# Kernel optimization log

Measured on AMD Instinct MI355X. Metric: run time of the kernel, lower is better.

Reference implementation:

```python
import jax, jax.numpy as jnp
import numpy as np

EPS = 1e-5

def layer_norm(x, g, b):
    mu = jnp.mean(x, axis=-1, keepdims=True)
    var = jnp.mean(jnp.square(x - mu), axis=-1, keepdims=True)
    return (x - mu) * jax.lax.rsqrt(var + EPS) * g + b

def setup_inputs() -> dict:
    key = jax.random.key(0)
    ks = jax.random.split(key, 16)
    B, S, D, H, T = 8, 1024, 512, 8, 6
    Dff = 4 * D
    s = 0.02
    return {
        "x": jax.random.normal(ks[0], (B, S, D), jnp.float32),
        "signal_type_ids": jax.random.randint(ks[1], (B, S), 0, T, jnp.int32),
        "emb": jax.random.normal(ks[2], (T, D), jnp.float32) * s,
        "in_proj_w": jax.random.normal(ks[3], (3 * D, D), jnp.float32) * s,
        "in_proj_b": jnp.zeros((3 * D,), jnp.float32),
        "out_proj_w": jax.random.normal(ks[4], (D, D), jnp.float32) * s,
        "out_proj_b": jnp.zeros((D,), jnp.float32),
        "ln1_g": jnp.ones((D,), jnp.float32),
        "ln1_b": jnp.zeros((D,), jnp.float32),
        "ln2_g": jnp.ones((D,), jnp.float32),
        "ln2_b": jnp.zeros((D,), jnp.float32),
        "w1": jax.random.normal(ks[5], (Dff, D), jnp.float32) * s,
        "b1": jnp.zeros((Dff,), jnp.float32),
        "w2": jax.random.normal(ks[6], (D, Dff), jnp.float32) * s,
        "b2": jnp.zeros((D,), jnp.float32),
    }

def reference(x, signal_type_ids, emb, in_proj_w, in_proj_b, out_proj_w, out_proj_b,
              ln1_g, ln1_b, ln2_g, ln2_b, w1, b1, w2, b2):
    B, S, D = x.shape
    H = 8
    hd = D // H
    # embedding add
    x = x + emb[signal_type_ids]
    # pre-norm MHA (need_weights=True path, average_attn_weights=True)
    xn = layer_norm(x, ln1_g, ln1_b)
    qkv = xn @ in_proj_w.T + in_proj_b            # [B,S,3D]
    q, k, v = jnp.split(qkv, 3, axis=-1)
    q = q.reshape(B, S, H, hd)
    k = k.reshape(B, S, H, hd)
    v = v.reshape(B, S, H, hd)
    scores = jnp.einsum("bqhd,bkhd->bhqk", q, k) / jnp.sqrt(jnp.asarray(hd, x.dtype))
    attn = jax.nn.softmax(scores, axis=-1)        # [B,H,S,S]
    attn_weights = jnp.mean(attn, axis=1)         # averaged over heads [B,S,S]
    ctx = jnp.einsum("bhqk,bkhd->bqhd", attn, v).reshape(B, S, D)
    attn_out = ctx @ out_proj_w.T + out_proj_b
    x = x + attn_out
    # FFN with exact GELU (torch nn.GELU default)
    h = layer_norm(x, ln2_g, ln2_b)
    h = jax.nn.gelu(h @ w1.T + b1, approximate=False)
    x = x + h @ w2.T + b2
    return x, attn_weights
```

## Files before the change

### kernel.cpp

```cpp
#include <hip/hip_runtime.h>
#include <math.h>

constexpr int CB = 8;
constexpr int CS = 1024;
constexpr int CD = 512;
constexpr int CH = 8;
constexpr int CHD = 64;
constexpr int CDFF = 2048;
constexpr int NROW = CB * CS;

typedef unsigned short u16;
typedef unsigned int u32;
typedef __attribute__((ext_vector_type(8))) short short8;
typedef __attribute__((ext_vector_type(8))) unsigned short ushort8v;
typedef __attribute__((ext_vector_type(4))) float floatx4;

__device__ inline u16 f2bf(float f) {
    union { float f; unsigned u; } v; v.f = f;
    unsigned u = v.u + 0x7FFFu + ((v.u >> 16) & 1u);
    return (u16)(u >> 16);
}
__device__ inline float bf2f(u16 h) {
    union { unsigned u; float f; } v; v.u = ((unsigned)h) << 16;
    return v.f;
}

__device__ inline float gelu_fast(float v) {
    float u = v * (1.0f + 0.044715f * v * v);
    float e = __expf(-1.5957691216057308f * u);
    return v / (1.0f + e);
}

__device__ inline void gload16(const u16* g, u16* l) {
    __builtin_amdgcn_global_load_lds(
        (const __attribute__((address_space(1))) u32*)g,
        (__attribute__((address_space(3))) u32*)l, 16, 0, 0);
}

__device__ inline void barrier_raw() {
    asm volatile("" ::: "memory");
    __builtin_amdgcn_s_barrier();
    asm volatile("" ::: "memory");
}

__global__ __launch_bounds__(256) void ln_kernel(
    const float* __restrict__ x, const int* __restrict__ ids,
    const float* __restrict__ emb,
    const float* __restrict__ g, const float* __restrict__ beta,
    float* __restrict__ xr_out, u16* __restrict__ xn_out)
{
    __shared__ float red1[4], red2[4];
    __shared__ float mu_s, ri_s;
    int row = blockIdx.x;
    int tid = threadIdx.x;
    int d0 = tid * 2;
    const float* xrow = x + (size_t)row * CD;
    float2 xv = *(const float2*)(xrow + d0);
    float v0 = xv.x, v1 = xv.y;
    if (emb) {
        int id = ids[row];
        float2 ev = *(const float2*)(emb + (size_t)id * CD + d0);
        v0 += ev.x; v1 += ev.y;
    }
    float s1 = v0 + v1;
    float s2 = v0 * v0 + v1 * v1;
    for (int off = 32; off > 0; off >>= 1) {
        s1 += __shfl_down(s1, off, 64);
        s2 += __shfl_down(s2, off, 64);
    }
    int wave = tid >> 6;
    if ((tid & 63) == 0) { red1[wave] = s1; red2[wave] = s2; }
    __syncthreads();
    if (tid == 0) {
        float t1 = red1[0] + red1[1] + red1[2] + red1[3];
        float t2 = red2[0] + red2[1] + red2[2] + red2[3];
        float mu = t1 / CD;
        float var = t2 / CD - mu * mu;
        mu_s = mu;
        ri_s = rsqrtf(var + 1e-5f);
    }
    __syncthreads();
    float mu = mu_s, ri = ri_s;
    if (xr_out) {
        float2 o; o.x = v0; o.y = v1;
        *(float2*)(xr_out + (size_t)row * CD + d0) = o;
    }
    float2 gv = *(const float2*)(g + d0);
    float2 bv = *(const float2*)(beta + d0);
    float n0 = (v0 - mu) * ri * gv.x + bv.x;
    float n1 = (v1 - mu) * ri * gv.y + bv.y;
    u32 pk = (u32)f2bf(n0) | ((u32)f2bf(n1) << 16);
    *(u32*)(xn_out + (size_t)row * CD + d0) = pk;
}

__global__ __launch_bounds__(256) void conv4_kernel(
    const float* __restrict__ s0, const float* __restrict__ s1,
    const float* __restrict__ s2, const float* __restrict__ s3,
    u16* __restrict__ dst)
{
    size_t i = ((size_t)blockIdx.x * 256 + threadIdx.x) * 8;
    const float* src;
    size_t off;
    if (i < 786432)        { src = s0; off = i; }
    else if (i < 1048576)  { src = s1; off = i - 786432; }
    else if (i < 2097152)  { src = s2; off = i - 1048576; }
    else                   { src = s3; off = i - 2097152; }
    float4 a = *(const float4*)(src + off);
    float4 b = *(const float4*)(src + off + 4);
    ushort8v o;
    o[0] = f2bf(a.x); o[1] = f2bf(a.y); o[2] = f2bf(a.z); o[3] = f2bf(a.w);
    o[4] = f2bf(b.x); o[5] = f2bf(b.y); o[6] = f2bf(b.z); o[7] = f2bf(b.w);
    *(ushort8v*)(dst + i) = o;
}

template <int ACT, int RES, int OUTBF>
__global__ __launch_bounds__(256) void gemm_mfma(
    const u16* __restrict__ A, const u16* __restrict__ W,
    const float* __restrict__ bias, const float* __restrict__ res,
    void* __restrict__ Cout, int M, int N, int K)
{
    __shared__ u16 As[2][128 * 32];
    __shared__ u16 Bs[2][128 * 32];
    int t = threadIdx.x;
    int lane = t & 63;
    int w = t >> 6;
    int m0 = blockIdx.x * 128;
    int n0 = blockIdx.y * 128;
    int col = lane & 15;
    int quad = lane >> 4;
    int wm = w & 1, wn = w >> 1;
    int lo = w * 512;

    const u16* ag = A + (size_t)(m0 + (t >> 2)) * K + (t & 3) * 8;
    const u16* ag2 = ag + (size_t)64 * K;
    const u16* bg = W + (size_t)(n0 + (t >> 2)) * K + (t & 3) * 8;
    const u16* bg2 = bg + (size_t)64 * K;

    gload16(ag, As[0] + lo);
    gload16(ag2, As[0] + 2048 + lo);
    gload16(bg, Bs[0] + lo);
    gload16(bg2, Bs[0] + 2048 + lo);
    gload16(ag + 32, As[1] + lo);
    gload16(ag2 + 32, As[1] + 2048 + lo);
    gload16(bg + 32, Bs[1] + lo);
    gload16(bg2 + 32, Bs[1] + 2048 + lo);

    floatx4 acc[4][4];
#pragma unroll
    for (int i = 0; i < 4; i++)
#pragma unroll
        for (int j = 0; j < 4; j++) acc[i][j] = (floatx4){0.f, 0.f, 0.f, 0.f};

    int nk = K >> 5;
    for (int kt = 0; kt < nk; kt++) {
        int cur = kt & 1;
        if (kt == nk - 1) asm volatile("s_waitcnt vmcnt(0)" ::: "memory");
        else              asm volatile("s_waitcnt vmcnt(4)" ::: "memory");
        barrier_raw();
        short8 af[4], bf[4];
#pragma unroll
        for (int mi = 0; mi < 4; mi++)
            af[mi] = *(const short8*)&As[cur][(wm * 64 + mi * 16 + col) * 32 + quad * 8];
#pragma unroll
        for (int ni = 0; ni < 4; ni++)
            bf[ni] = *(const short8*)&Bs[cur][(wn * 64 + ni * 16 + col) * 32 + quad * 8];
#pragma unroll
        for (int mi = 0; mi < 4; mi++)
#pragma unroll
            for (int ni = 0; ni < 4; ni++)
                acc[mi][ni] = __builtin_amdgcn_mfma_f32_16x16x32_bf16(
                    af[mi], bf[ni], acc[mi][ni], 0, 0, 0);
        barrier_raw();
        if (kt + 2 < nk) {
            int ko = (kt + 2) * 32;
            gload16(ag + ko, As[cur] + lo);
            gload16(ag2 + ko, As[cur] + 2048 + lo);
            gload16(bg + ko, Bs[cur] + lo);
            gload16(bg2 + ko, Bs[cur] + 2048 + lo);
        }
    }

#pragma unroll
    for (int mi = 0; mi < 4; mi++)
#pragma unroll
        for (int ni = 0; ni < 4; ni++) {
            int c = n0 + wn * 64 + ni * 16 + col;
            float bv = bias[c];
#pragma unroll
            for (int r = 0; r < 4; r++) {
                int m = m0 + wm * 64 + mi * 16 + quad * 4 + r;
                float v = acc[mi][ni][r] + bv;
                if (ACT == 1) v = gelu_fast(v);
                if (RES) v += res[(size_t)m * N + c];
                if (OUTBF) ((u16*)Cout)[(size_t)m * N + c] = f2bf(v);
                else       ((float*)Cout)[(size_t)m * N + c] = v;
            }
        }
}

template <int ACT, int RES, int OUTBF>
__global__ __launch_bounds__(256) void gemm_mfma64(
    const u16* __restrict__ A, const u16* __restrict__ W,
    const float* __restrict__ bias, const float* __restrict__ res,
    void* __restrict__ Cout, int M, int N, int K)
{
    __shared__ u16 As[2][64 * 32];
    __shared__ u16 Bs[2][128 * 32];
    int t = threadIdx.x;
    int lane = t & 63;
    int w = t >> 6;
    int m0 = blockIdx.x * 64;
    int n0 = blockIdx.y * 128;
    int col = lane & 15;
    int quad = lane >> 4;
    int lo = w * 512;

    const u16* ag = A + (size_t)(m0 + (t >> 2)) * K + (t & 3) * 8;
    const u16* bg = W + (size_t)(n0 + (t >> 2)) * K + (t & 3) * 8;
    const u16* bg2 = bg + (size_t)64 * K;

    gload16(ag, As[0] + lo);
    gload16(bg, Bs[0] + lo);
    gload16(bg2, Bs[0] + 2048 + lo);
    gload16(ag + 32, As[1] + lo);
    gload16(bg + 32, Bs[1] + lo);
    gload16(bg2 + 32, Bs[1] + 2048 + lo);

    floatx4 acc[4][2];
#pragma unroll
    for (int i = 0; i < 4; i++)
#pragma unroll
        for (int j = 0; j < 2; j++) acc[i][j] = (floatx4){0.f, 0.f, 0.f, 0.f};

    int nk = K >> 5;
    for (int kt = 0; kt < nk; kt++) {
        int cur = kt & 1;
        if (kt == nk - 1) asm volatile("s_waitcnt vmcnt(0)" ::: "memory");
        else              asm volatile("s_waitcnt vmcnt(3)" ::: "memory");
        barrier_raw();
        short8 af[4], bf[2];
#pragma unroll
        for (int mi = 0; mi < 4; mi++)
            af[mi] = *(const short8*)&As[cur][(mi * 16 + col) * 32 + quad * 8];
#pragma unroll
        for (int ni = 0; ni < 2; ni++)
            bf[ni] = *(const short8*)&Bs[cur][(w * 32 + ni * 16 + col) * 32 + quad * 8];
#pragma unroll
        for (int mi = 0; mi < 4; mi++)
#pragma unroll
            for (int ni = 0; ni < 2; ni++)
                acc[mi][ni] = __builtin_amdgcn_mfma_f32_16x16x32_bf16(
                    af[mi], bf[ni], acc[mi][ni], 0, 0, 0);
        barrier_raw();
        if (kt + 2 < nk) {
            int ko = (kt + 2) * 32;
            gload16(ag + ko, As[cur] + lo);
            gload16(bg + ko, Bs[cur] + lo);
            gload16(bg2 + ko, Bs[cur] + 2048 + lo);
        }
    }

#pragma unroll
    for (int mi = 0; mi < 4; mi++)
#pragma unroll
        for (int ni = 0; ni < 2; ni++) {
            int c = n0 + w * 32 + ni * 16 + col;
            float bv = bias[c];
#pragma unroll
            for (int r = 0; r < 4; r++) {
                int m = m0 + mi * 16 + quad * 4 + r;
                float v = acc[mi][ni][r] + bv;
                if (ACT == 1) v = gelu_fast(v);
                if (RES) v += res[(size_t)m * N + c];
                if (OUTBF) ((u16*)Cout)[(size_t)m * N + c] = f2bf(v);
                else       ((float*)Cout)[(size_t)m * N + c] = v;
            }
        }
}

__global__ __launch_bounds__(256) void vt_kernel(
    const u16* __restrict__ qkvb, u16* __restrict__ vt)
{
    __shared__ u16 tile[64][72];
    int b = blockIdx.x >> 4;
    int s0 = (blockIdx.x & 15) * 64;
    int h = blockIdx.y;
    int t = threadIdx.x;
    int r = t >> 2;
    int c0 = (t & 3) * 16;
    const u16* src = qkvb + (size_t)(b * CS + s0 + r) * 1536 + 2 * CD + h * CHD + c0;
    *(ushort8v*)&tile[r][c0] = *(const ushort8v*)src;
    *(ushort8v*)&tile[r][c0 + 8] = *(const ushort8v*)(src + 8);
    __syncthreads();
    u16* dst = vt + (((size_t)b * CH + h) * CHD + r) * CS + s0 + c0;
    ushort8v lo, hi;
#pragma unroll
    for (int j = 0; j < 8; j++) { lo[j] = tile[c0 + j][r]; hi[j] = tile[c0 + 8 + j][r]; }
    *(ushort8v*)dst = lo;
    *(ushort8v*)(dst + 8) = hi;
}

__global__ __launch_bounds__(256, 2) void attn_fused_kernel(
    const u16* __restrict__ qkvb, const u16* __restrict__ vt,
    u16* __restrict__ Se, float* __restrict__ Lout,
    u16* __restrict__ ctx, int b0)
{
    __shared__ u16 Qs[2][64 * 32];
    __shared__ u16 Ks[2][2][64 * 32];
    __shared__ u16 Vs[2][2][64 * 32];
    __shared__ u16 S[64][72];
    __shared__ float rs[4][4][16];

    int t = threadIdx.x;
    int lane = t & 63;
    int w = t >> 6;
    int col = lane & 15;
    int quad = lane >> 4;
    int bid = blockIdx.x;
    int xcd = bid & 7;
    int j = bid >> 3;
    int bhl = xcd * 4 + (j >> 4);
    int qt = j & 15;
    int lb = bhl >> 3, h = bhl & 7;
    int b = b0 + lb;
    int q0 = qt * 64;
    int bh = b * CH + h;
    size_t splane = (size_t)(lb * CH + h) * CS * CS;

    int srow = t >> 2;
    int scol = (t & 3) * 8;

    const u16* ksrc0 = qkvb + (size_t)(b * CS + srow) * 1536 + CD + h * CHD + scol;
    const u16* vsrc0 = vt + ((size_t)bh * CHD + srow) * CS + scol;

    {
        const u16* qsrc = qkvb + (size_t)(b * CS + q0 + srow) * 1536 + h * CHD + scol;
        gload16(qsrc, Qs[0] + w * 512);
        gload16(qsrc + 32, Qs[1] + w * 512);
        gload16(ksrc0, Ks[0][0] + w * 512);
        gload16(ksrc0 + 32, Ks[0][1] + w * 512);
        gload16(vsrc0, Vs[0][0] + w * 512);
        gload16(vsrc0 + 32, Vs[0][1] + w * 512);
    }
    __syncthreads();

    short8 qf[2][4];
#pragma unroll
    for (int dsl = 0; dsl < 2; dsl++)
#pragma unroll
        for (int nq = 0; nq < 4; nq++)
            qf[dsl][nq] = *(const short8*)&Qs[dsl][(nq * 16 + col) * 32 + quad * 8];

    floatx4 acc[4];
#pragma unroll
    for (int i = 0; i < 4; i++) acc[i] = (floatx4){0.f, 0.f, 0.f, 0.f};
    float esum[4] = {0.f, 0.f, 0.f, 0.f};

    for (int kc = 0; kc < 16; kc++) {
        int cur = kc & 1;
        short8 kf0 = *(const short8*)&Ks[cur][0][(w * 16 + col) * 32 + quad * 8];
        short8 kf1 = *(const short8*)&Ks[cur][1][(w * 16 + col) * 32 + quad * 8];
#pragma unroll
        for (int nq = 0; nq < 4; nq++) {
            floatx4 c = {0.f, 0.f, 0.f, 0.f};
            c = __builtin_amdgcn_mfma_f32_16x16x32_bf16(kf0, qf[0][nq], c, 0, 0, 0);
            c = __builtin_amdgcn_mfma_f32_16x16x32_bf16(kf1, qf[1][nq], c, 0, 0, 0);
            float e0 = __expf(c[0] * 0.125f);
            float e1 = __expf(c[1] * 0.125f);
            float e2 = __expf(c[2] * 0.125f);
            float e3 = __expf(c[3] * 0.125f);
            esum[nq] += (e0 + e1) + (e2 + e3);
            union { float f; u32 u; } a0, a1, a2, a3;
            a0.f = e0; a1.f = e1; a2.f = e2; a3.f = e3;
            u32 p0 = (a0.u >> 16) | (a1.u & 0xFFFF0000u);
            u32 p1 = (a2.u >> 16) | (a3.u & 0xFFFF0000u);
            u32* sp = (u32*)&S[nq * 16 + col][w * 16 + quad * 4];
            sp[0] = p0; sp[1] = p1;
            u32* gp = (u32*)(Se + splane + (size_t)(q0 + nq * 16 + col) * CS
                             + kc * 64 + w * 16 + quad * 4);
            gp[0] = p0; gp[1] = p1;
        }
        __syncthreads();

        if (kc < 15) {
            int ko = (kc + 1) * 64;
            const u16* ks = ksrc0 + (size_t)ko * 1536;
            gload16(ks, Ks[cur ^ 1][0] + w * 512);
            gload16(ks + 32, Ks[cur ^ 1][1] + w * 512);
            gload16(vsrc0 + ko, Vs[cur ^ 1][0] + w * 512);
            gload16(vsrc0 + ko + 32, Vs[cur ^ 1][1] + w * 512);
        }

        short8 sf0 = *(const short8*)&S[w * 16 + col][quad * 8];
        short8 sf1 = *(const short8*)&S[w * 16 + col][32 + quad * 8];
#pragma unroll
        for (int nd = 0; nd < 4; nd++) {
            short8 vf0 = *(const short8*)&Vs[cur][0][(nd * 16 + col) * 32 + quad * 8];
            short8 vf1 = *(const short8*)&Vs[cur][1][(nd * 16 + col) * 32 + quad * 8];
            acc[nd] = __builtin_amdgcn_mfma_f32_16x16x32_bf16(sf0, vf0, acc[nd], 0, 0, 0);
            acc[nd] = __builtin_amdgcn_mfma_f32_16x16x32_bf16(sf1, vf1, acc[nd], 0, 0, 0);
        }
        __syncthreads();
    }

#pragma unroll
    for (int nq = 0; nq < 4; nq++) {
        float v = esum[nq];
        v += __shfl_xor(v, 16, 64);
        v += __shfl_xor(v, 32, 64);
        if (quad == 0) rs[w][nq][col] = v;
    }
    __syncthreads();
    if (t < 64) {
        int nq = t >> 4, c2 = t & 15;
        float L = rs[0][nq][c2] + rs[1][nq][c2] + rs[2][nq][c2] + rs[3][nq][c2];
        Lout[((size_t)bh << 10) + q0 + nq * 16 + c2] = L;
    }

    float li[4];
#pragma unroll
    for (int r = 0; r < 4; r++) {
        int cr = quad * 4 + r;
        li[r] = 1.0f / (rs[0][w][cr] + rs[1][w][cr] + rs[2][w][cr] + rs[3][w][cr]);
    }
    u16* cb = ctx + ((size_t)(b * CS) + q0 + w * 16 + quad * 4) * CD + h * CHD + col;
#pragma unroll
    for (int nd = 0; nd < 4; nd++)
#pragma unroll
        for (int r = 0; r < 4; r++)
            cb[(size_t)r * CD + nd * 16] = f2bf(acc[nd][r] * li[r]);
}

__global__ __launch_bounds__(256, 8) void attn_aw_kernel(
    const u16* __restrict__ Se, const float* __restrict__ Lin,
    float* __restrict__ aw_out, int b0)
{
    int bq = blockIdx.x;
    int bl = bq >> 9;
    int b = b0 + bl;
    int q = (bq & 511) * 2 + (threadIdx.x >> 7);
    int k0 = (threadIdx.x & 127) * 8;

    float acc[8];
#pragma unroll
    for (int i = 0; i < 8; i++) acc[i] = 0.f;

#pragma unroll
    for (int h = 0; h < CH; h++) {
        float linv = 0.125f / Lin[(((size_t)(b * CH + h)) << 10) + q];
        const u16* sp = Se + ((size_t)(bl * CH + h) * CS + q) * CS + k0;
        ushort8v e = *(const ushort8v*)sp;
#pragma unroll
        for (int i = 0; i < 8; i++) acc[i] += bf2f(e[i]) * linv;
    }
    float* ap = aw_out + ((size_t)(b * CS) + q) * CS + k0;
    *(float4*)ap = make_float4(acc[0], acc[1], acc[2], acc[3]);
    *(float4*)(ap + 4) = make_float4(acc[4], acc[5], acc[6], acc[7]);
}

extern "C" void kernel_launch(void* const* d_in, const int* in_sizes, int n_in,
                              void* d_out, int out_size, void* d_ws, size_t ws_size,
                              hipStream_t stream)
{
    const float* x    = (const float*)d_in[0];
    const int*   ids  = (const int*)d_in[1];
    const float* emb  = (const float*)d_in[2];
    const float* inw  = (const float*)d_in[3];
    const float* inb  = (const float*)d_in[4];
    const float* ow   = (const float*)d_in[5];
    const float* ob   = (const float*)d_in[6];
    const float* g1   = (const float*)d_in[7];
    const float* be1  = (const float*)d_in[8];
    const float* g2   = (const float*)d_in[9];
    const float* be2  = (const float*)d_in[10];
    const float* w1   = (const float*)d_in[11];
    const float* b1   = (const float*)d_in[12];
    const float* w2   = (const float*)d_in[13];
    const float* b2   = (const float*)d_in[14];

    float* out_x  = (float*)d_out;
    float* out_aw = out_x + (size_t)CB * CS * CD;

    char* p = (char*)d_ws;
    float* xr   = (float*)p; p += (size_t)NROW * CD * 4;
    float* x2   = (float*)p; p += (size_t)NROW * CD * 4;
    u16* xnb    = (u16*)p;   p += (size_t)NROW * CD * 2;
    u16* qkvb   = (u16*)p;   p += (size_t)NROW * 3 * CD * 2;
    u16* ctxb   = (u16*)p;   p += (size_t)NROW * CD * 2;
    u16* hidb   = (u16*)p;   p += (size_t)NROW * CDFF * 2;
    u16* inwb   = (u16*)p;   p += (size_t)3 * CD * CD * 2;
    u16* owb    = (u16*)p;   p += (size_t)CD * CD * 2;
    u16* w1b    = (u16*)p;   p += (size_t)CDFF * CD * 2;
    u16* w2b    = (u16*)p;   p += (size_t)CD * CDFF * 2;
    float* Lbuf = (float*)p; p += (size_t)CB * CH * CS * 4;
    u16* Se     = (u16*)p;   p += (size_t)(CB / 2) * CH * CS * CS * 2;

    u16* vtb = hidb;

    dim3 blk(256);
    conv4_kernel<<<(3 * CD * CD + CD * CD + 2 * CDFF * CD) / 2048, blk, 0, stream>>>(
        inw, ow, w1, w2, inwb);
    ln_kernel<<<NROW, blk, 0, stream>>>(x, ids, emb, g1, be1, xr, xnb);
    gemm_mfma<0, 0, 1><<<dim3(NROW / 128, (3 * CD) / 128), blk, 0, stream>>>(
        xnb, inwb, inb, nullptr, qkvb, NROW, 3 * CD, CD);
    vt_kernel<<<dim3(CB * (CS / 64), CH), blk, 0, stream>>>(qkvb, vtb);
    for (int half = 0; half < 2; half++) {
        int b0 = half * 4;
        attn_fused_kernel<<<512, blk, 0, stream>>>(qkvb, vtb, Se, Lbuf, ctxb, b0);
        attn_aw_kernel<<<2048, blk, 0, stream>>>(Se, Lbuf, out_aw, b0);
    }
    gemm_mfma64<0, 1, 0><<<dim3(NROW / 64, CD / 128), blk, 0, stream>>>(
        ctxb, owb, ob, xr, x2, NROW, CD, CD);
    ln_kernel<<<NROW, blk, 0, stream>>>(x2, nullptr, nullptr, g2, be2, nullptr, xnb);
    gemm_mfma<1, 0, 1><<<dim3(NROW / 128, CDFF / 128), blk, 0, stream>>>(
        xnb, w1b, b1, nullptr, hidb, NROW, CDFF, CD);
    gemm_mfma64<0, 1, 0><<<dim3(NROW / 64, CD / 128), blk, 0, stream>>>(
        hidb, w2b, b2, x2, out_x, NROW, CD, CDFF);
}
```

Before: 319.0 us.

## Swizzle LDS tiles with XOR chunk permutation and triple-buffer GEMM loads

Global-to-LDS loads now place each 16-byte chunk at an XOR-permuted column (chunk index XOR row bits), and the MFMA fragment reads use the matching swizzle. This targets LDS bank conflicts in the GEMM and attention kernels. The GEMM kernels also move from double to triple buffering, issuing loads three k-steps ahead with adjusted vmcnt waits to hide more global latency. The cost is extra LDS per block, which may reduce occupancy.

```diff
diff --git a/kernel.cpp b/kernel.cpp
--- a/kernel.cpp
+++ b/kernel.cpp
@@ -42,6 +42,8 @@
     __builtin_amdgcn_s_barrier();
     asm volatile("" ::: "memory");
 }
+
+#define SRC_CHUNK(t) ((((t) & 3) ^ (((t) >> 3) & 3)) * 8)
 
 __global__ __launch_bounds__(256) void ln_kernel(
     const float* __restrict__ x, const int* __restrict__ ids,
@@ -119,8 +121,8 @@
     const float* __restrict__ bias, const float* __restrict__ res,
     void* __restrict__ Cout, int M, int N, int K)
 {
-    __shared__ u16 As[2][128 * 32];
-    __shared__ u16 Bs[2][128 * 32];
+    __shared__ u16 As[3][128 * 32];
+    __shared__ u16 Bs[3][128 * 32];
     int t = threadIdx.x;
     int lane = t & 63;
     int w = t >> 6;
@@ -130,20 +132,20 @@
     int quad = lane >> 4;
     int wm = w & 1, wn = w >> 1;
     int lo = w * 512;
-
-    const u16* ag = A + (size_t)(m0 + (t >> 2)) * K + (t & 3) * 8;
+    int qs8 = (quad ^ ((col >> 1) & 3)) * 8;
+
+    const u16* ag = A + (size_t)(m0 + (t >> 2)) * K + SRC_CHUNK(t);
     const u16* ag2 = ag + (size_t)64 * K;
-    const u16* bg = W + (size_t)(n0 + (t >> 2)) * K + (t & 3) * 8;
+    const u16* bg = W + (size_t)(n0 + (t >> 2)) * K + SRC_CHUNK(t);
     const u16* bg2 = bg + (size_t)64 * K;
 
-    gload16(ag, As[0] + lo);
-    gload16(ag2, As[0] + 2048 + lo);
-    gload16(bg, Bs[0] + lo);
-    gload16(bg2, Bs[0] + 2048 + lo);
-    gload16(ag + 32, As[1] + lo);
-    gload16(ag2 + 32, As[1] + 2048 + lo);
-    gload16(bg + 32, Bs[1] + lo);
-    gload16(bg2 + 32, Bs[1] + 2048 + lo);
+#pragma unroll
+    for (int i = 0; i < 3; i++) {
+        gload16(ag + i * 32, As[i] + lo);
+        gload16(ag2 + i * 32, As[i] + 2048 + lo);
+        gload16(bg + i * 32, Bs[i] + lo);
+        gload16(bg2 + i * 32, Bs[i] + 2048 + lo);
+    }
 
     floatx4 acc[4][4];
 #pragma unroll
@@ -153,17 +155,18 @@
 
     int nk = K >> 5;
     for (int kt = 0; kt < nk; kt++) {
-        int cur = kt & 1;
-        if (kt == nk - 1) asm volatile("s_waitcnt vmcnt(0)" ::: "memory");
-        else              asm volatile("s_waitcnt vmcnt(4)" ::: "memory");
+        int cur = kt % 3;
+        if (kt < nk - 2)       asm volatile("s_waitcnt vmcnt(8)" ::: "memory");
+        else if (kt == nk - 2) asm volatile("s_waitcnt vmcnt(4)" ::: "memory");
+        else                   asm volatile("s_waitcnt vmcnt(0)" ::: "memory");
         barrier_raw();
         short8 af[4], bf[4];
 #pragma unroll
         for (int mi = 0; mi < 4; mi++)
-            af[mi] = *(const short8*)&As[cur][(wm * 64 + mi * 16 + col) * 32 + quad * 8];
+            af[mi] = *(const short8*)&As[cur][(wm * 64 + mi * 16 + col) * 32 + qs8];
 #pragma unroll
         for (int ni = 0; ni < 4; ni++)
-            bf[ni] = *(const short8*)&Bs[cur][(wn * 64 + ni * 16 + col) * 32 + quad * 8];
+            bf[ni] = *(const short8*)&Bs[cur][(wn * 64 + ni * 16 + col) * 32 + qs8];
 #pragma unroll
         for (int mi = 0; mi < 4; mi++)
 #pragma unroll
@@ -171,8 +174,8 @@
                 acc[mi][ni] = __builtin_amdgcn_mfma_f32_16x16x32_bf16(
                     af[mi], bf[ni], acc[mi][ni], 0, 0, 0);
         barrier_raw();
-        if (kt + 2 < nk) {
-            int ko = (kt + 2) * 32;
+        if (kt + 3 < nk) {
+            int ko = (kt + 3) * 32;
             gload16(ag + ko, As[cur] + lo);
             gload16(ag2 + ko, As[cur] + 2048 + lo);
             gload16(bg + ko, Bs[cur] + lo);
@@ -204,8 +207,8 @@
     const float* __restrict__ bias, const float* __restrict__ res,
     void* __restrict__ Cout, int M, int N, int K)
 {
-    __shared__ u16 As[2][64 * 32];
-    __shared__ u16 Bs[2][128 * 32];
+    __shared__ u16 As[3][64 * 32];
+    __shared__ u16 Bs[3][128 * 32];
     int t = threadIdx.x;
     int lane = t & 63;
     int w = t >> 6;
@@ -214,17 +217,18 @@
     int col = lane & 15;
     int quad = lane >> 4;
     int lo = w * 512;
-
-    const u16* ag = A + (size_t)(m0 + (t >> 2)) * K + (t & 3) * 8;
-    const u16* bg = W + (size_t)(n0 + (t >> 2)) * K + (t & 3) * 8;
+    int qs8 = (quad ^ ((col >> 1) & 3)) * 8;
+
+    const u16* ag = A + (size_t)(m0 + (t >> 2)) * K + SRC_CHUNK(t);
+    const u16* bg = W + (size_t)(n0 + (t >> 2)) * K + SRC_CHUNK(t);
     const u16* bg2 = bg + (size_t)64 * K;
 
-    gload16(ag, As[0] + lo);
-    gload16(bg, Bs[0] + lo);
-    gload16(bg2, Bs[0] + 2048 + lo);
-    gload16(ag + 32, As[1] + lo);
-    gload16(bg + 32, Bs[1] + lo);
-    gload16(bg2 + 32, Bs[1] + 2048 + lo);
+#pragma unroll
+    for (int i = 0; i < 3; i++) {
+        gload16(ag + i * 32, As[i] + lo);
+        gload16(bg + i * 32, Bs[i] + lo);
+        gload16(bg2 + i * 32, Bs[i] + 2048 + lo);
+    }
 
     floatx4 acc[4][2];
 #pragma unroll
@@ -234,17 +238,18 @@
 
     int nk = K >> 5;
     for (int kt = 0; kt < nk; kt++) {
-        int cur = kt & 1;
-        if (kt == nk - 1) asm volatile("s_waitcnt vmcnt(0)" ::: "memory");
-        else              asm volatile("s_waitcnt vmcnt(3)" ::: "memory");
+        int cur = kt % 3;
+        if (kt < nk - 2)       asm volatile("s_waitcnt vmcnt(6)" ::: "memory");
+        else if (kt == nk - 2) asm volatile("s_waitcnt vmcnt(3)" ::: "memory");
+        else                   asm volatile("s_waitcnt vmcnt(0)" ::: "memory");
         barrier_raw();
         short8 af[4], bf[2];
 #pragma unroll
         for (int mi = 0; mi < 4; mi++)
-            af[mi] = *(const short8*)&As[cur][(mi * 16 + col) * 32 + quad * 8];
+            af[mi] = *(const short8*)&As[cur][(mi * 16 + col) * 32 + qs8];
 #pragma unroll
         for (int ni = 0; ni < 2; ni++)
-            bf[ni] = *(const short8*)&Bs[cur][(w * 32 + ni * 16 + col) * 32 + quad * 8];
+            bf[ni] = *(const short8*)&Bs[cur][(w * 32 + ni * 16 + col) * 32 + qs8];
 #pragma unroll
         for (int mi = 0; mi < 4; mi++)
 #pragma unroll
@@ -252,8 +257,8 @@
                 acc[mi][ni] = __builtin_amdgcn_mfma_f32_16x16x32_bf16(
                     af[mi], bf[ni], acc[mi][ni], 0, 0, 0);
         barrier_raw();
-        if (kt + 2 < nk) {
-            int ko = (kt + 2) * 32;
+        if (kt + 3 < nk) {
+            int ko = (kt + 3) * 32;
             gload16(ag + ko, As[cur] + lo);
             gload16(bg + ko, Bs[cur] + lo);
             gload16(bg2 + ko, Bs[cur] + 2048 + lo);
@@ -316,6 +321,7 @@
     int w = t >> 6;
     int col = lane & 15;
     int quad = lane >> 4;
+    int qs8 = (quad ^ ((col >> 1) & 3)) * 8;
     int bid = blockIdx.x;
     int xcd = bid & 7;
     int j = bid >> 3;
@@ -328,7 +334,7 @@
     size_t splane = (size_t)(lb * CH + h) * CS * CS;
 
     int srow = t >> 2;
-    int scol = (t & 3) * 8;
+    int scol = SRC_CHUNK(t);
 
     const u16* ksrc0 = qkvb + (size_t)(b * CS + srow) * 1536 + CD + h * CHD + scol;
     const u16* vsrc0 = vt + ((size_t)bh * CHD + srow) * CS + scol;
@@ -349,7 +355,7 @@
     for (int dsl = 0; dsl < 2; dsl++)
 #pragma unroll
         for (int nq = 0; nq < 4; nq++)
-            qf[dsl][nq] = *(const short8*)&Qs[dsl][(nq * 16 + col) * 32 + quad * 8];
+            qf[dsl][nq] = *(const short8*)&Qs[dsl][(nq * 16 + col) * 32 + qs8];
 
     floatx4 acc[4];
 #pragma unroll
@@ -358,8 +364,8 @@
 
     for (int kc = 0; kc < 16; kc++) {
         int cur = kc & 1;
-        short8 kf0 = *(const short8*)&Ks[cur][0][(w * 16 + col) * 32 + quad * 8];
-        short8 kf1 = *(const short8*)&Ks[cur][1][(w * 16 + col) * 32 + quad * 8];
+        short8 kf0 = *(const short8*)&Ks[cur][0][(w * 16 + col) * 32 + qs8];
+        short8 kf1 = *(const short8*)&Ks[cur][1][(w * 16 + col) * 32 + qs8];
 #pragma unroll
         for (int nq = 0; nq < 4; nq++) {
             floatx4 c = {0.f, 0.f, 0.f, 0.f};
@@ -395,8 +401,8 @@
         short8 sf1 = *(const short8*)&S[w * 16 + col][32 + quad * 8];
 #pragma unroll
         for (int nd = 0; nd < 4; nd++) {
-            short8 vf0 = *(const short8*)&Vs[cur][0][(nd * 16 + col) * 32 + quad * 8];
-            short8 vf1 = *(const short8*)&Vs[cur][1][(nd * 16 + col) * 32 + quad * 8];
+            short8 vf0 = *(const short8*)&Vs[cur][0][(nd * 16 + col) * 32 + qs8];
+            short8 vf1 = *(const short8*)&Vs[cur][1][(nd * 16 + col) * 32 + qs8];
             acc[nd] = __builtin_amdgcn_mfma_f32_16x16x32_bf16(sf0, vf0, acc[nd], 0, 0, 0);
             acc[nd] = __builtin_amdgcn_mfma_f32_16x16x32_bf16(sf1, vf1, acc[nd], 0, 0, 0);
         }
```

Result: faster. 309.1 us (-3.1%).
